# Optimization experiments

Measured on AMD Instinct MI355X. Metric: run time of the kernel, lower is better.

## Reference

```python
import jax, jax.numpy as jnp
import numpy as np

N_NODES = 100000
N_EDGES = 1600000
IN, HID, OUT = 128, 128, 64


def setup_inputs() -> dict:
    key = jax.random.key(0)
    ks = jax.random.split(key, 6)
    features = jax.random.normal(ks[0], (N_NODES, IN), dtype=jnp.float32)
    src = jax.random.randint(ks[1], (N_EDGES,), 0, N_NODES)
    dst = jax.random.randint(ks[2], (N_EDGES,), 0, N_NODES)
    # Glorot-style init scales
    W1 = jax.random.normal(ks[3], (IN, HID), dtype=jnp.float32) * (1.0 / np.sqrt(IN))
    b1 = jnp.zeros((HID,), dtype=jnp.float32)
    W2 = jax.random.normal(ks[4], (HID, OUT), dtype=jnp.float32) * (1.0 / np.sqrt(HID))
    b2 = jnp.zeros((OUT,), dtype=jnp.float32)
    return {"features": features, "src": src, "dst": dst,
            "W1": W1, "b1": b1, "W2": W2, "b2": b2}


def _graph_conv(h, W, b, src, dst, deg_inv):
    # DGL GraphConv, norm='right': aggregate sum of (x_u W) over in-neighbors,
    # divide by in-degree (clamped to >=1), then add bias.
    m = h @ W                                   # [N, F_out]
    agg = jax.ops.segment_sum(m[src], dst, num_segments=h.shape[0])  # [N, F_out]
    return agg * deg_inv[:, None] + b


def reference(features, src, dst, W1, b1, W2, b2):
    n = features.shape[0]
    deg = jax.ops.segment_sum(jnp.ones_like(dst, dtype=features.dtype), dst,
                              num_segments=n)
    deg_inv = 1.0 / jnp.maximum(deg, 1.0)       # clamp(min=1) as in DGL
    h = jax.nn.relu(_graph_conv(features, W1, b1, src, dst, deg_inv))
    # dropout(0.5) is identity in eval mode
    out = _graph_conv(h, W2, b2, src, dst, deg_inv)
    return out
```

## Files before the change

kernel.cpp:

```cpp
#include <hip/hip_runtime.h>
#include <hip/hip_fp16.h>


constexpr int CAP = 6144;
constexpr int CHUNK = 8192;

typedef _Float16 f16x8 __attribute__((ext_vector_type(8)));
typedef float f32x4 __attribute__((ext_vector_type(4)));

__global__ __launch_bounds__(256) void k_prep(
    const int* __restrict__ dst, int* __restrict__ bcnt,
    const float* __restrict__ X, __half* __restrict__ X16,
    const float* __restrict__ W1, const float* __restrict__ W2,
    __half* __restrict__ W1t, __half* __restrict__ W2t,
    int E, int NB, long long n4)
{
    __shared__ int sh[1024];
    const int tid = threadIdx.x;
    if (blockIdx.x < 256) {
        for (int i = tid; i < NB; i += 256) sh[i] = 0;
        __syncthreads();
        for (int e = blockIdx.x * 256 + tid; e < E; e += 256 * 256)
            atomicAdd(&sh[dst[e] >> 7], 1);
        __syncthreads();
        for (int i = tid; i < NB; i += 256) {
            const int v = sh[i];
            if (v) atomicAdd(&bcnt[i], v);
        }
    } else if (blockIdx.x < 352) {
        const int t = (blockIdx.x - 256) * 256 + tid;
        if (t < 128 * 128) {
            const int k = t >> 7, n = t & 127;
            W1t[n * 128 + k] = __float2half(W1[t]);
        } else {
            const int u = t - 128 * 128;
            const int k = u >> 6, n = u & 63;
            W2t[n * 128 + k] = __float2half(W2[u]);
        }
    }
    for (long long i = (long long)blockIdx.x * 256 + tid; i < n4;
         i += (long long)gridDim.x * 256) {
        const float4 v = ((const float4*)X)[i];
        __half2 h0 = __floats2half2_rn(v.x, v.y);
        __half2 h1 = __floats2half2_rn(v.z, v.w);
        uint2 o;
        o.x = *(const unsigned*)&h0;
        o.y = *(const unsigned*)&h1;
        ((uint2*)X16)[i] = o;
    }
}

__global__ __launch_bounds__(1024) void k_bscan(
    const int* __restrict__ bcnt, int* __restrict__ bstart,
    int* __restrict__ bcursor, int NB, int E)
{
    __shared__ int sh[1024];
    const int t = threadIdx.x;
    const int v = (t < NB) ? bcnt[t] : 0;
    sh[t] = v;
    __syncthreads();
    for (int off = 1; off < 1024; off <<= 1) {
        int u = (t >= off) ? sh[t - off] : 0;
        __syncthreads();
        if (t >= off) sh[t] += u;
        __syncthreads();
    }
    if (t < NB) {
        const int ex = sh[t] - v;
        bstart[t] = ex;
        bcursor[t] = ex;
    }
    if (t == 0) bstart[NB] = E;
}

__global__ __launch_bounds__(256) void k_binscatter(
    const int* __restrict__ src, const int* __restrict__ dst,
    int* __restrict__ bcursor, unsigned* __restrict__ pairs, int E, int NB)
{
    __shared__ int hist[1024];
    __shared__ int base[1024];
    const int b0 = blockIdx.x * CHUNK;
    const int cnt = min(CHUNK, E - b0);
    const int tid = threadIdx.x;

    for (int i = tid; i < NB; i += 256) hist[i] = 0;
    __syncthreads();
    for (int i = tid; i < cnt; i += 256)
        atomicAdd(&hist[dst[b0 + i] >> 7], 1);
    __syncthreads();
    for (int i = tid; i < NB; i += 256) {
        const int c = hist[i];
        base[i] = c ? atomicAdd(&bcursor[i], c) : 0;
    }
    __syncthreads();
    int i = tid;
    for (; i + 768 < cnt; i += 1024) {
        const int d0 = dst[b0 + i], s0 = src[b0 + i];
        const int d1 = dst[b0 + i + 256], s1 = src[b0 + i + 256];
        const int d2 = dst[b0 + i + 512], s2 = src[b0 + i + 512];
        const int d3 = dst[b0 + i + 768], s3 = src[b0 + i + 768];
        const int p0 = atomicAdd(&base[d0 >> 7], 1);
        const int p1 = atomicAdd(&base[d1 >> 7], 1);
        const int p2 = atomicAdd(&base[d2 >> 7], 1);
        const int p3 = atomicAdd(&base[d3 >> 7], 1);
        pairs[p0] = (unsigned)s0 | ((unsigned)(d0 & 127) << 17);
        pairs[p1] = (unsigned)s1 | ((unsigned)(d1 & 127) << 17);
        pairs[p2] = (unsigned)s2 | ((unsigned)(d2 & 127) << 17);
        pairs[p3] = (unsigned)s3 | ((unsigned)(d3 & 127) << 17);
    }
    for (; i < cnt; i += 256) {
        const int d = dst[b0 + i];
        const int p = atomicAdd(&base[d >> 7], 1);
        pairs[p] = (unsigned)src[b0 + i] | ((unsigned)(d & 127) << 17);
    }
}

__global__ __launch_bounds__(256) void k_sort(
    const unsigned* __restrict__ pairs, const int* __restrict__ bstart,
    int* __restrict__ edge_src, int* __restrict__ row_start, int N, int E)
{
    __shared__ unsigned sp[CAP];
    __shared__ int sorted[CAP];
    __shared__ int lcnt[128];
    __shared__ int ls[128];
    const int b = blockIdx.x;
    const int tid = threadIdx.x;
    const int beg = bstart[b], end = bstart[b + 1];
    const int cnt = end - beg;
    const bool fits = (cnt <= CAP);

    if (tid < 128) lcnt[tid] = 0;
    __syncthreads();

    if (fits) {
        for (int i = tid; i < cnt; i += 256) {
            const unsigned p = pairs[beg + i];
            sp[i] = p;
            atomicAdd(&lcnt[p >> 17], 1);
        }
    } else {
        for (int i = tid; i < cnt; i += 256)
            atomicAdd(&lcnt[pairs[beg + i] >> 17], 1);
    }
    __syncthreads();

    if (tid < 128) ls[tid] = lcnt[tid];
    __syncthreads();
    for (int off = 1; off < 128; off <<= 1) {
        int v = 0;
        if (tid < 128 && tid >= off) v = ls[tid - off];
        __syncthreads();
        if (tid < 128 && tid >= off) ls[tid] += v;
        __syncthreads();
    }

    if (tid < 128) {
        const int node = b * 128 + tid;
        if (node <= N) row_start[node] = beg + ls[tid] - lcnt[tid];
    }
    if (b == 0 && tid == 0) row_start[N] = E;
    __syncthreads();

    if (tid < 128) ls[tid] -= lcnt[tid];
    __syncthreads();

    if (fits) {
        for (int i = tid; i < cnt; i += 256) {
            const unsigned p = sp[i];
            const int pos = atomicAdd(&ls[p >> 17], 1);
            sorted[pos] = (int)(p & 0x1FFFFu);
        }
        __syncthreads();
        for (int i = tid; i < cnt; i += 256) edge_src[beg + i] = sorted[i];
    } else {
        for (int i = tid; i < cnt; i += 256) {
            const unsigned p = pairs[beg + i];
            const int pos = atomicAdd(&ls[p >> 17], 1);
            edge_src[beg + pos] = (int)(p & 0x1FFFFu);
        }
    }
}

__global__ __launch_bounds__(256) void k_agg1(
    const __half* __restrict__ M, const int* __restrict__ edge_src,
    const int* __restrict__ row_start, __half* __restrict__ outp, int N)
{
    const int node = (blockIdx.x * 256 + threadIdx.x) >> 4;
    if (node >= N) return;
    const unsigned li = threadIdx.x & 15;
    const int beg = row_start[node];
    const int end = row_start[node + 1];
    const float inv = 1.0f / fmaxf((float)(end - beg), 1.0f);
    const uint4* M4 = (const uint4*)M;

    float acc[8] = {};
    int j = beg;
    for (; j + 7 < end; j += 8) {
        unsigned o[8];
#pragma unroll
        for (int q = 0; q < 8; ++q)
            o[q] = ((unsigned)edge_src[j + q] << 4) | li;
        uint4 v[8];
#pragma unroll
        for (int q = 0; q < 8; ++q) v[q] = M4[o[q]];
#pragma unroll
        for (int q = 0; q < 8; ++q) {
            const __half2* h = (const __half2*)&v[q];
#pragma unroll
            for (int p = 0; p < 4; ++p) {
                const float2 f = __half22float2(h[p]);
                acc[2 * p] += f.x;
                acc[2 * p + 1] += f.y;
            }
        }
    }
    for (; j < end; ++j) {
        const uint4 v = M4[((unsigned)edge_src[j] << 4) | li];
        const __half2* h = (const __half2*)&v;
#pragma unroll
        for (int p = 0; p < 4; ++p) {
            const float2 f = __half22float2(h[p]);
            acc[2 * p] += f.x;
            acc[2 * p + 1] += f.y;
        }
    }
    __half2 r[4];
#pragma unroll
    for (int p = 0; p < 4; ++p)
        r[p] = __floats2half2_rn(acc[2 * p] * inv, acc[2 * p + 1] * inv);
    ((uint4*)(outp + (size_t)node * 128))[li] = *(const uint4*)r;
}

__global__ __launch_bounds__(256) void k_agg2(
    const __half* __restrict__ M, const int* __restrict__ edge_src,
    const int* __restrict__ row_start, const float* __restrict__ bias,
    float* __restrict__ outp, int N)
{
    const int node = (blockIdx.x * 256 + threadIdx.x) >> 3;
    if (node >= N) return;
    const unsigned li = threadIdx.x & 7;
    const int beg = row_start[node];
    const int end = row_start[node + 1];
    const float inv = 1.0f / fmaxf((float)(end - beg), 1.0f);
    const uint4* M4 = (const uint4*)M;

    float acc[8] = {};
    int j = beg;
    for (; j + 7 < end; j += 8) {
        unsigned o[8];
#pragma unroll
        for (int q = 0; q < 8; ++q)
            o[q] = ((unsigned)edge_src[j + q] << 3) | li;
        uint4 v[8];
#pragma unroll
        for (int q = 0; q < 8; ++q) v[q] = M4[o[q]];
#pragma unroll
        for (int q = 0; q < 8; ++q) {
            const __half2* h = (const __half2*)&v[q];
#pragma unroll
            for (int p = 0; p < 4; ++p) {
                const float2 f = __half22float2(h[p]);
                acc[2 * p] += f.x;
                acc[2 * p + 1] += f.y;
            }
        }
    }
    for (; j < end; ++j) {
        const uint4 v = M4[((unsigned)edge_src[j] << 3) | li];
        const __half2* h = (const __half2*)&v;
#pragma unroll
        for (int p = 0; p < 4; ++p) {
            const float2 f = __half22float2(h[p]);
            acc[2 * p] += f.x;
            acc[2 * p + 1] += f.y;
        }
    }
    const float4 b0 = ((const float4*)bias)[li * 2];
    const float4 b1 = ((const float4*)bias)[li * 2 + 1];
    float4 o0, o1;
    o0.x = fmaf(acc[0], inv, b0.x);
    o0.y = fmaf(acc[1], inv, b0.y);
    o0.z = fmaf(acc[2], inv, b0.z);
    o0.w = fmaf(acc[3], inv, b0.w);
    o1.x = fmaf(acc[4], inv, b1.x);
    o1.y = fmaf(acc[5], inv, b1.y);
    o1.z = fmaf(acc[6], inv, b1.z);
    o1.w = fmaf(acc[7], inv, b1.w);
    float4* op = (float4*)(outp + (size_t)node * 64);
    op[li * 2] = o0;
    op[li * 2 + 1] = o1;
}

__global__ __launch_bounds__(256) void k_mgemm2(
    const __half* __restrict__ A, const __half* __restrict__ W1t,
    const float* __restrict__ b1, const __half* __restrict__ W2t,
    __half* __restrict__ C, int N)
{
    __shared__ __align__(16) char lds[16384];
    const int tid = threadIdx.x;
    const int row0 = blockIdx.x * 64;

    for (int i = tid; i < 1024; i += 256) {
        const int r = i >> 4, ch = i & 15;
        const int row = row0 + r;
        uint4 v = make_uint4(0, 0, 0, 0);
        if (row < N) v = *(const uint4*)(A + (size_t)row * 128 + ch * 8);
        *(uint4*)(lds + r * 256 + ((ch * 16) ^ ((r & 7) << 4))) = v;
    }
    __syncthreads();

    const int w = tid >> 6, l = tid & 63;
    const int lr = l & 15, lk = l >> 4;
    const int arow = w * 16 + lr;

    f32x4 acc1[8] = {};
#pragma unroll
    for (int kb = 0; kb < 4; ++kb) {
        const f16x8 a = *(const f16x8*)(lds + arow * 256 +
                                        ((kb * 64 + lk * 16) ^ ((arow & 7) << 4)));
#pragma unroll
        for (int nt = 0; nt < 8; ++nt) {
            const f16x8 b = *(const f16x8*)(W1t + (nt * 16 + lr) * 128 + kb * 32 + lk * 8);
            acc1[nt] = __builtin_amdgcn_mfma_f32_16x16x32_f16(a, b, acc1[nt], 0, 0, 0);
        }
    }
    __syncthreads();

    char* hw = lds + w * 4096;
#pragma unroll
    for (int nt = 0; nt < 8; ++nt) {
        const int col = nt * 16 + lr;
        const float bv = b1[col];
#pragma unroll
        for (int i = 0; i < 4; ++i) {
            const int r = lk * 4 + i;
            const float v = fmaxf(acc1[nt][i] + bv, 0.f);
            *(__half*)(hw + r * 256 + ((col * 2) ^ ((r & 7) << 4))) = __float2half(v);
        }
    }
    __syncthreads();

    f32x4 acc2[4] = {};
#pragma unroll
    for (int kb = 0; kb < 4; ++kb) {
        const f16x8 a2 = *(const f16x8*)(hw + lr * 256 +
                                         ((kb * 64 + lk * 16) ^ ((lr & 7) << 4)));
#pragma unroll
        for (int nt = 0; nt < 4; ++nt) {
            const f16x8 b = *(const f16x8*)(W2t + (nt * 16 + lr) * 128 + kb * 32 + lk * 8);
            acc2[nt] = __builtin_amdgcn_mfma_f32_16x16x32_f16(a2, b, acc2[nt], 0, 0, 0);
        }
    }
    __syncthreads();

#pragma unroll
    for (int nt = 0; nt < 4; ++nt) {
        const int col = nt * 16 + lr;
#pragma unroll
        for (int i = 0; i < 4; ++i) {
            const int r = lk * 4 + i;
            *(__half*)(hw + r * 128 + ((col * 2) ^ ((r & 7) << 4))) = __float2half(acc2[nt][i]);
        }
    }
    __syncthreads();

    const int rbase = row0 + w * 16;
    for (int i = l; i < 128; i += 64) {
        const int r = i >> 3, c = i & 7;
        const int row = rbase + r;
        if (row < N)
            *(uint4*)(C + (size_t)row * 64 + c * 8) =
                *(const uint4*)(hw + r * 128 + ((c * 16) ^ ((r & 7) << 4)));
    }
}

extern "C" void kernel_launch(void* const* d_in, const int* in_sizes, int n_in,
                              void* d_out, int out_size, void* d_ws, size_t ws_size,
                              hipStream_t stream)
{
    const float* X  = (const float*)d_in[0];
    const int*  src = (const int*)d_in[1];
    const int*  dst = (const int*)d_in[2];
    const float* W1 = (const float*)d_in[3];
    const float* b1 = (const float*)d_in[4];
    const float* W2 = (const float*)d_in[5];
    const float* b2 = (const float*)d_in[6];
    float* out = (float*)d_out;

    const int N = in_sizes[0] / 128;
    const int E = in_sizes[1];
    const int NB = (N + 127) / 128;

    __half* X16   = (__half*)d_ws;
    __half* agg1h = X16 + (size_t)N * 128;
    __half* scr   = agg1h + (size_t)N * 128;
    __half* m2h   = X16;
    unsigned* pairs = (unsigned*)scr;
    int* edge_src  = (int*)(scr + (size_t)N * 128);
    int* row_start = edge_src + E;
    int* bcnt      = row_start + N + 1;
    int* bstart    = bcnt + NB;
    int* bcursor   = bstart + NB + 1;
    __half* W1t    = (__half*)(bcursor + NB);
    __half* W2t    = W1t + 128 * 128;

    hipMemsetAsync(bcnt, 0, (size_t)NB * sizeof(int), stream);

    k_prep<<<2048, 256, 0, stream>>>(dst, bcnt, X, X16, W1, W2, W1t, W2t,
                                     E, NB, (long long)N * 32);
    k_bscan<<<1, 1024, 0, stream>>>(bcnt, bstart, bcursor, NB, E);
    k_binscatter<<<(E + CHUNK - 1) / CHUNK, 256, 0, stream>>>(src, dst, bcursor, pairs, E, NB);
    k_sort<<<NB, 256, 0, stream>>>(pairs, bstart, edge_src, row_start, N, E);

    k_agg1<<<(N * 16 + 255) / 256, 256, 0, stream>>>(X16, edge_src, row_start, agg1h, N);
    k_mgemm2<<<(N + 63) / 64, 256, 0, stream>>>(agg1h, W1t, b1, W2t, m2h, N);
    k_agg2<<<(N * 8 + 255) / 256, 256, 0, stream>>>(m2h, edge_src, row_start, b2, out, N);
}
```

Baseline: 218.4 us.

## Replace atomic bin cursors with per-chunk histograms and column prefix scan

```diff
diff --git a/kernel.cpp b/kernel.cpp
--- a/kernel.cpp
+++ b/kernel.cpp
@@ -3,32 +3,32 @@
 
 
 constexpr int CAP = 6144;
-constexpr int CHUNK = 8192;
+constexpr int CHUNK = 4096;
 
 typedef _Float16 f16x8 __attribute__((ext_vector_type(8)));
 typedef float f32x4 __attribute__((ext_vector_type(4)));
 
 __global__ __launch_bounds__(256) void k_prep(
-    const int* __restrict__ dst, int* __restrict__ bcnt,
+    const int* __restrict__ dst, int* __restrict__ counts,
     const float* __restrict__ X, __half* __restrict__ X16,
     const float* __restrict__ W1, const float* __restrict__ W2,
     __half* __restrict__ W1t, __half* __restrict__ W2t,
-    int E, int NB, long long n4)
+    int E, int NB, int NC, long long n4)
 {
     __shared__ int sh[1024];
     const int tid = threadIdx.x;
-    if (blockIdx.x < 256) {
+    if (blockIdx.x < NC) {
+        const int c = blockIdx.x;
+        const int b0 = c * CHUNK;
+        const int cnt = min(CHUNK, E - b0);
         for (int i = tid; i < NB; i += 256) sh[i] = 0;
         __syncthreads();
-        for (int e = blockIdx.x * 256 + tid; e < E; e += 256 * 256)
-            atomicAdd(&sh[dst[e] >> 7], 1);
-        __syncthreads();
-        for (int i = tid; i < NB; i += 256) {
-            const int v = sh[i];
-            if (v) atomicAdd(&bcnt[i], v);
-        }
-    } else if (blockIdx.x < 352) {
-        const int t = (blockIdx.x - 256) * 256 + tid;
+        for (int i = tid; i < cnt; i += 256)
+            atomicAdd(&sh[dst[b0 + i] >> 7], 1);
+        __syncthreads();
+        for (int i = tid; i < NB; i += 256) counts[(size_t)c * NB + i] = sh[i];
+    } else if (blockIdx.x < NC + 96) {
+        const int t = (blockIdx.x - NC) * 256 + tid;
         if (t < 128 * 128) {
             const int k = t >> 7, n = t & 127;
             W1t[n * 128 + k] = __float2half(W1[t]);
@@ -50,13 +50,39 @@
     }
 }
 
+__global__ __launch_bounds__(256) void k_colscan(
+    int* __restrict__ counts, int* __restrict__ btot, int NB, int NC)
+{
+    __shared__ int sh[256];
+    const int b = blockIdx.x;
+    const int tid = threadIdx.x;
+    int carry = 0;
+    for (int t0 = 0; t0 < NC; t0 += 256) {
+        const int idx = t0 + tid;
+        const int v = (idx < NC) ? counts[(size_t)idx * NB + b] : 0;
+        sh[tid] = v;
+        __syncthreads();
+        for (int off = 1; off < 256; off <<= 1) {
+            int u = (tid >= off) ? sh[tid - off] : 0;
+            __syncthreads();
+            if (tid >= off) sh[tid] += u;
+            __syncthreads();
+        }
+        const int incl = sh[tid];
+        const int tile_total = sh[255];
+        if (idx < NC) counts[(size_t)idx * NB + b] = incl - v + carry;
+        carry += tile_total;
+        __syncthreads();
+    }
+    if (tid == 0) btot[b] = carry;
+}
+
 __global__ __launch_bounds__(1024) void k_bscan(
-    const int* __restrict__ bcnt, int* __restrict__ bstart,
-    int* __restrict__ bcursor, int NB, int E)
+    const int* __restrict__ btot, int* __restrict__ bstart, int NB, int E)
 {
     __shared__ int sh[1024];
     const int t = threadIdx.x;
-    const int v = (t < NB) ? bcnt[t] : 0;
+    const int v = (t < NB) ? btot[t] : 0;
     sh[t] = v;
     __syncthreads();
     for (int off = 1; off < 1024; off <<= 1) {
@@ -65,44 +91,35 @@
         if (t >= off) sh[t] += u;
         __syncthreads();
     }
-    if (t < NB) {
-        const int ex = sh[t] - v;
-        bstart[t] = ex;
-        bcursor[t] = ex;
-    }
+    if (t < NB) bstart[t] = sh[t] - v;
     if (t == 0) bstart[NB] = E;
 }
 
-__global__ __launch_bounds__(256) void k_binscatter(
+__global__ __launch_bounds__(256) void k_scatter2(
     const int* __restrict__ src, const int* __restrict__ dst,
-    int* __restrict__ bcursor, unsigned* __restrict__ pairs, int E, int NB)
-{
-    __shared__ int hist[1024];
-    __shared__ int base[1024];
-    const int b0 = blockIdx.x * CHUNK;
+    const int* __restrict__ cbase, const int* __restrict__ bstart,
+    unsigned* __restrict__ pairs, int E, int NB)
+{
+    __shared__ int cur[1024];
+    const int c = blockIdx.x;
+    const int b0 = c * CHUNK;
     const int cnt = min(CHUNK, E - b0);
     const int tid = threadIdx.x;
 
-    for (int i = tid; i < NB; i += 256) hist[i] = 0;
-    __syncthreads();
-    for (int i = tid; i < cnt; i += 256)
-        atomicAdd(&hist[dst[b0 + i] >> 7], 1);
-    __syncthreads();
-    for (int i = tid; i < NB; i += 256) {
-        const int c = hist[i];
-        base[i] = c ? atomicAdd(&bcursor[i], c) : 0;
-    }
-    __syncthreads();
+    for (int i = tid; i < NB; i += 256)
+        cur[i] = bstart[i] + cbase[(size_t)c * NB + i];
+    __syncthreads();
+
     int i = tid;
     for (; i + 768 < cnt; i += 1024) {
         const int d0 = dst[b0 + i], s0 = src[b0 + i];
         const int d1 = dst[b0 + i + 256], s1 = src[b0 + i + 256];
         const int d2 = dst[b0 + i + 512], s2 = src[b0 + i + 512];
         const int d3 = dst[b0 + i + 768], s3 = src[b0 + i + 768];
-        const int p0 = atomicAdd(&base[d0 >> 7], 1);
-        const int p1 = atomicAdd(&base[d1 >> 7], 1);
-        const int p2 = atomicAdd(&base[d2 >> 7], 1);
-        const int p3 = atomicAdd(&base[d3 >> 7], 1);
+        const int p0 = atomicAdd(&cur[d0 >> 7], 1);
+        const int p1 = atomicAdd(&cur[d1 >> 7], 1);
+        const int p2 = atomicAdd(&cur[d2 >> 7], 1);
+        const int p3 = atomicAdd(&cur[d3 >> 7], 1);
         pairs[p0] = (unsigned)s0 | ((unsigned)(d0 & 127) << 17);
         pairs[p1] = (unsigned)s1 | ((unsigned)(d1 & 127) << 17);
         pairs[p2] = (unsigned)s2 | ((unsigned)(d2 & 127) << 17);
@@ -110,7 +127,7 @@
     }
     for (; i < cnt; i += 256) {
         const int d = dst[b0 + i];
-        const int p = atomicAdd(&base[d >> 7], 1);
+        const int p = atomicAdd(&cur[d >> 7], 1);
         pairs[p] = (unsigned)src[b0 + i] | ((unsigned)(d & 127) << 17);
     }
 }
@@ -390,6 +407,7 @@
     const int N = in_sizes[0] / 128;
     const int E = in_sizes[1];
     const int NB = (N + 127) / 128;
+    const int NC = (E + CHUNK - 1) / CHUNK;
 
     __half* X16   = (__half*)d_ws;
     __half* agg1h = X16 + (size_t)N * 128;
@@ -398,18 +416,17 @@
     unsigned* pairs = (unsigned*)scr;
     int* edge_src  = (int*)(scr + (size_t)N * 128);
     int* row_start = edge_src + E;
-    int* bcnt      = row_start + N + 1;
-    int* bstart    = bcnt + NB;
-    int* bcursor   = bstart + NB + 1;
-    __half* W1t    = (__half*)(bcursor + NB);
+    int* bstart    = row_start + N + 1;
+    int* btot      = bstart + NB + 1;
+    int* counts    = btot + NB;
+    __half* W1t    = (__half*)(counts + (size_t)NC * NB);
     __half* W2t    = W1t + 128 * 128;
 
-    hipMemsetAsync(bcnt, 0, (size_t)NB * sizeof(int), stream);
-
-    k_prep<<<2048, 256, 0, stream>>>(dst, bcnt, X, X16, W1, W2, W1t, W2t,
-                                     E, NB, (long long)N * 32);
-    k_bscan<<<1, 1024, 0, stream>>>(bcnt, bstart, bcursor, NB, E);
-    k_binscatter<<<(E + CHUNK - 1) / CHUNK, 256, 0, stream>>>(src, dst, bcursor, pairs, E, NB);
+    k_prep<<<2048, 256, 0, stream>>>(dst, counts, X, X16, W1, W2, W1t, W2t,
+                                     E, NB, NC, (long long)N * 32);
+    k_colscan<<<NB, 256, 0, stream>>>(counts, btot, NB, NC);
+    k_bscan<<<1, 1024, 0, stream>>>(btot, bstart, NB, E);
+    k_scatter2<<<NC, 256, 0, stream>>>(src, dst, counts, bstart, pairs, E, NB);
     k_sort<<<NB, 256, 0, stream>>>(pairs, bstart, edge_src, row_start, N, E);
 
     k_agg1<<<(N * 16 + 255) / 256, 256, 0, stream>>>(X16, edge_src, row_start, agg1h, N);
```

Result: faster. 200.2 us (-8.3%).
